# Kernel optimization log

Hardware: AMD Instinct MI355X
Metric: run time of the kernel (lower is better)

The kernel has to match this reference:

```python
import jax, jax.numpy as jnp
import numpy as np

WS = 3          # window_size == patch size (asserted in the torch forward)
R = WS // 2
V = WS ** 3     # 27 voxels per patch == window length
D_MODEL = 256
HEADS = 8
LAYERS = 3

_IDX = np.arange(WS)[:, None] + np.arange(WS)[None, :]  # [WS, WS] sliding-window indices into padded grid


def _layer_norm(x, g, b, eps=1e-5):
    mu = jnp.mean(x, axis=-1, keepdims=True)
    var = jnp.var(x, axis=-1, keepdims=True)
    return (x - mu) * jax.lax.rsqrt(var + eps) * g + b


def _gather_windows(x):
    # x: [B, WS, WS, WS, C] -> zero-padded 3x3x3 neighborhoods, [B*V, V, C]
    xp = jnp.pad(x, ((0, 0), (R, R), (R, R), (R, R), (0, 0)))
    nb = xp[:, _IDX][:, :, :, _IDX][:, :, :, :, :, _IDX]
    # axes: [B, d_ctr, d_win, h_ctr, h_win, w_ctr, w_win, C]
    nb = nb.transpose(0, 1, 3, 5, 2, 4, 6, 7)
    return nb.reshape(x.shape[0] * V, V, x.shape[-1])


def _window_mask(known_mask):
    # boundary (padding) positions -> False; interior -> known_mask value
    mp = jnp.pad(known_mask, ((0, 0), (R, R), (R, R), (R, R)))
    m = mp[:, _IDX][:, :, :, _IDX][:, :, :, :, :, _IDX]
    m = m.transpose(0, 1, 3, 5, 2, 4, 6)
    return m.reshape(known_mask.shape[0] * V, V)


def _forward(neighbors_patch, known_mask, w_in, b_in, pos_embed,
             ln1_g, ln1_b, ln2_g, ln2_b,
             Wq, bq, Wk, bk, Wv, bv, Wo, bo,
             W1, b1, W2, b2, w_out, b_out):
    B = neighbors_patch.shape[0]
    d = w_in.shape[0]
    hd = d // HEADS
    scale = hd ** -0.5
    # Conv3d(1, d, kernel_size=1) == per-voxel affine scalar -> d channels; then +pos_embed
    x = neighbors_patch[:, 0, :, :, :, None] * w_in + b_in + pos_embed  # [B,WS,WS,WS,d]
    mask = _window_mask(known_mask)  # [B*V, V] (constant across layers)
    N = B * V
    t = x.reshape(N, d)
    for l in range(LAYERS):
        # NOTE: K/V come from RAW (un-normed) neighbor embeddings, Q from norm1(target) - as in the torch code
        nb = _gather_windows(t.reshape(B, WS, WS, WS, d))  # [N, V, d]
        tn = _layer_norm(t, ln1_g[l], ln1_b[l])
        q = (tn @ Wq[l] + bq[l]).reshape(N, HEADS, hd)
        k = (nb @ Wk[l] + bk[l]).reshape(N, V, HEADS, hd)
        v = (nb @ Wv[l] + bv[l]).reshape(N, V, HEADS, hd)
        s = jnp.einsum('nhd,nlhd->nhl', q, k) * scale
        s = jnp.where(mask[:, None, :], s, -1e30)
        # fully-masked rows: torch softmax gives NaN then zeroed; here uniform*mask -> 0, same result
        a = jax.nn.softmax(s, axis=-1) * mask[:, None, :]
        o = jnp.einsum('nhl,nlhd->nhd', a, v).reshape(N, d) @ Wo[l] + bo[l]
        t = t + o  # dropout is identity in eval
        tn2 = _layer_norm(t, ln2_g[l], ln2_b[l])
        h = jax.nn.gelu(tn2 @ W1[l] + b1[l], approximate=False)
        t = t + h @ W2[l] + b2[l]
    center = t.reshape(B, WS, WS, WS, d)[:, R, R, R, :]
    return (center @ w_out)[:, None] + b_out  # [B, 1]


def setup_inputs():
    key = jax.random.key(0)
    ks = jax.random.split(key, 24)
    B, d, L, ff = 256, D_MODEL, LAYERS, 4 * D_MODEL
    nrm = lambda k, shape, s=0.02: jax.random.normal(k, shape, jnp.float32) * s
    return {
        'neighbors_patch': (jax.random.uniform(ks[0], (B, 1, WS, WS, WS)) < 0.5).astype(jnp.float32),
        'known_mask': jax.random.randint(ks[1], (B, WS, WS, WS), 0, 2).astype(bool),
        'w_in': nrm(ks[2], (d,), 0.5), 'b_in': nrm(ks[3], (d,)),
        'pos_embed': nrm(ks[4], (WS, WS, WS, d)),
        'ln1_g': jnp.ones((L, d)), 'ln1_b': jnp.zeros((L, d)),
        'ln2_g': jnp.ones((L, d)), 'ln2_b': jnp.zeros((L, d)),
        'Wq': nrm(ks[5], (L, d, d)), 'bq': nrm(ks[6], (L, d)),
        'Wk': nrm(ks[7], (L, d, d)), 'bk': nrm(ks[8], (L, d)),
        'Wv': nrm(ks[9], (L, d, d)), 'bv': nrm(ks[10], (L, d)),
        'Wo': nrm(ks[11], (L, d, d)), 'bo': nrm(ks[12], (L, d)),
        'W1': nrm(ks[13], (L, d, ff)), 'b1': nrm(ks[14], (L, ff)),
        'W2': nrm(ks[15], (L, ff, d)), 'b2': nrm(ks[16], (L, d)),
        'w_out': nrm(ks[17], (d,)), 'b_out': nrm(ks[18], (1,)),
    }


def reference(neighbors_patch, known_mask, w_in, b_in, pos_embed, ln1_g, ln1_b, ln2_g, ln2_b, Wq, bq, Wk, bk, Wv, bv, Wo, bo, W1, b1, W2, b2, w_out, b_out):
    return _forward(neighbors_patch, known_mask, w_in, b_in, pos_embed, ln1_g, ln1_b, ln2_g, ln2_b, Wq, bq, Wk, bk, Wv, bv, Wo, bo, W1, b1, W2, b2, w_out, b_out)
```

## Files before the change

### kernel.cpp

```cpp
#include <hip/hip_runtime.h>
#include <hip/hip_bf16.h>


#define NTOK 6912
#define DM   256
#define FF   1024

typedef __hip_bfloat16 bf16;
typedef __bf16 bf16x8 __attribute__((ext_vector_type(8)));
typedef float  f32x4  __attribute__((ext_vector_type(4)));

__device__ __forceinline__ void gload_lds16(const void* g, void* l) {
    __builtin_amdgcn_global_load_lds(
        (const __attribute__((address_space(1))) void*)g,
        (__attribute__((address_space(3))) void*)l, 16, 0, 0);
}

__device__ __forceinline__ unsigned short f2bf_bits(float x) {
    bf16 h = __float2bfloat16(x);
    union { bf16 h; unsigned short u; } c; c.h = h; return c.u;
}

__global__ __launch_bounds__(256) void embed_kernel(
    const float* __restrict__ npat, const float* __restrict__ w_in,
    const float* __restrict__ b_in, const float* __restrict__ pos,
    float* __restrict__ t, bf16* __restrict__ t_bf)
{
    int n = blockIdx.x;
    int c = threadIdx.x;
    int p = n % 27;
    float v = npat[n] * w_in[c] + b_in[c] + pos[p * DM + c];
    t[(size_t)n * DM + c] = v;
    t_bf[(size_t)n * DM + c] = __float2bfloat16(v);
}

__global__ void make_mask_kernel(const int* __restrict__ km,
                                 unsigned int* __restrict__ mask27)
{
    int n = blockIdx.x * blockDim.x + threadIdx.x;
    if (n >= NTOK) return;
    int b = n / 27, q = n % 27;
    int zq = q / 9, yq = (q / 3) % 3, xq = q % 3;
    unsigned int mb = 0u;
    for (int m = 0; m < 27; ++m) {
        int zm = m / 9, ym = (m / 3) % 3, xm = m % 3;
        if (abs(zm - zq) <= 1 && abs(ym - yq) <= 1 && abs(xm - xq) <= 1 &&
            km[b * 27 + m] != 0)
            mb |= (1u << m);
    }
    mask27[n] = mb;
}

__global__ __launch_bounds__(256) void convert_weights(
    const float* __restrict__ Wq, const float* __restrict__ Wk,
    const float* __restrict__ Wv, const float* __restrict__ Wo,
    const float* __restrict__ W1, const float* __restrict__ W2,
    bf16* __restrict__ Wt)
{
    __shared__ float tile[32][33];
    int id = blockIdx.z;
    int l = id / 6, wsel = id % 6;
    const float* src; bf16* dst; int K, N;
    if (wsel < 4) {
        const float* tbl[4] = {Wq, Wk, Wv, Wo};
        src = tbl[wsel] + (size_t)l * 65536; K = 256; N = 256;
        dst = Wt + (size_t)l * 786432 + wsel * 65536;
    } else if (wsel == 4) {
        src = W1 + (size_t)l * 262144; K = 256; N = 1024;
        dst = Wt + (size_t)l * 786432 + 262144;
    } else {
        src = W2 + (size_t)l * 262144; K = 1024; N = 256;
        dst = Wt + (size_t)l * 786432 + 524288;
    }
    int n0 = blockIdx.x * 32, k0 = blockIdx.y * 32;
    if (n0 >= N || k0 >= K) return;
    int tx = threadIdx.x, ty = threadIdx.y;
#pragma unroll
    for (int i = 0; i < 4; ++i)
        tile[ty + i * 8][tx] = src[(size_t)(k0 + ty + i * 8) * N + n0 + tx];
    __syncthreads();
#pragma unroll
    for (int i = 0; i < 4; ++i)
        dst[(size_t)(n0 + ty + i * 8) * K + k0 + tx] =
            __float2bfloat16(tile[tx][ty + i * 8]);
}

__global__ __launch_bounds__(256) void layernorm_kernel(
    const float* __restrict__ X, const float* __restrict__ g,
    const float* __restrict__ bta, bf16* __restrict__ Y)
{
    int n = blockIdx.x;
    int c = threadIdx.x;
    float x = X[(size_t)n * DM + c];
    float s = x, s2 = x * x;
    for (int off = 32; off; off >>= 1) {
        s  += __shfl_xor(s, off);
        s2 += __shfl_xor(s2, off);
    }
    __shared__ float ps[4], ps2[4];
    int w = c >> 6;
    if ((c & 63) == 0) { ps[w] = s; ps2[w] = s2; }
    __syncthreads();
    s  = ps[0] + ps[1] + ps[2] + ps[3];
    s2 = ps2[0] + ps2[1] + ps2[2] + ps2[3];
    float mu  = s * (1.0f / DM);
    float var = s2 * (1.0f / DM) - mu * mu;
    float r = rsqrtf(var + 1e-5f);
    Y[(size_t)n * DM + c] = __float2bfloat16((x - mu) * r * g[c] + bta[c]);
}

__device__ __forceinline__ void gemm_body(
    const bf16* __restrict__ A, const bf16* __restrict__ Bt,
    const float* __restrict__ bias, const float* __restrict__ residual,
    float* __restrict__ Cf, bf16* __restrict__ Cb,
    int K, int Nc, int act, int mode, int row0, int col0,
    bf16* As, bf16* Bs)
{
    int tid = threadIdx.x;
    int wv = tid >> 6, ln = tid & 63;
    int wr = wv >> 1, wc = wv & 1;

    f32x4 acc[4][2];
#pragma unroll
    for (int m = 0; m < 4; ++m)
#pragma unroll
        for (int n = 0; n < 2; ++n) acc[m][n] = (f32x4){0.f, 0.f, 0.f, 0.f};

    int lrow = ln >> 3;
    int kof  = (ln & 7) * 8;

    for (int k0 = 0; k0 < K; k0 += 64) {
        __syncthreads();
#pragma unroll
        for (int i = 0; i < 4; ++i) {
            int slot = i * 4 + wv;
            gload_lds16(A + (size_t)(row0 + slot * 8 + lrow) * K + k0 + kof,
                        As + slot * 512);
        }
#pragma unroll
        for (int i = 0; i < 2; ++i) {
            int slot = i * 4 + wv;
            gload_lds16(Bt + (size_t)(col0 + slot * 8 + lrow) * K + k0 + kof,
                        Bs + slot * 512);
        }
        __syncthreads();
        int lr = ln & 15, kg = ln >> 4;
#pragma unroll
        for (int kk = 0; kk < 2; ++kk) {
            int koff = kk * 32 + kg * 8;
            bf16x8 a[4], b[2];
#pragma unroll
            for (int m = 0; m < 4; ++m)
                a[m] = *(const bf16x8*)&As[(wr * 64 + m * 16 + lr) * 64 + koff];
#pragma unroll
            for (int n = 0; n < 2; ++n)
                b[n] = *(const bf16x8*)&Bs[(wc * 32 + n * 16 + lr) * 64 + koff];
#pragma unroll
            for (int m = 0; m < 4; ++m)
#pragma unroll
                for (int n = 0; n < 2; ++n)
                    acc[m][n] = __builtin_amdgcn_mfma_f32_16x16x32_bf16(
                        a[m], b[n], acc[m][n], 0, 0, 0);
        }
    }

    int lr = ln & 15, rg = ln >> 4;
#pragma unroll
    for (int m = 0; m < 4; ++m) {
#pragma unroll
        for (int n = 0; n < 2; ++n) {
            int col = col0 + wc * 32 + n * 16 + lr;
            float bcol = bias[col];
#pragma unroll
            for (int r = 0; r < 4; ++r) {
                int row = row0 + wr * 64 + m * 16 + rg * 4 + r;
                float v = acc[m][n][r] + bcol;
                if (mode == 2) {
                    int bb = row / 27, tok = row - bb * 27;
                    Cb[((size_t)bb * DM + col) * 32 + tok] = __float2bfloat16(v);
                } else {
                    size_t idx = (size_t)row * Nc + col;
                    if (residual) v += residual[idx];
                    if (act) v = 0.5f * v * (1.0f + erff(v * 0.70710678118654752f));
                    if (Cf) Cf[idx] = v;
                    if (Cb) Cb[idx] = __float2bfloat16(v);
                }
            }
        }
    }
}

__global__ __launch_bounds__(256) void gemm_bf16(
    const bf16* __restrict__ A, const bf16* __restrict__ Bt,
    const float* __restrict__ bias, const float* __restrict__ residual,
    float* __restrict__ Cf, bf16* __restrict__ Cb,
    int K, int Nc, int act)
{
    __shared__ __align__(16) bf16 As[128 * 64];
    __shared__ __align__(16) bf16 Bs[64 * 64];
    gemm_body(A, Bt, bias, residual, Cf, Cb, K, Nc, act, 0,
              blockIdx.x * 128, blockIdx.y * 64, As, Bs);
}

__global__ __launch_bounds__(256) void qkv_gemm(
    const bf16* __restrict__ tn, const bf16* __restrict__ tb,
    const bf16* __restrict__ wq,
    const float* __restrict__ bq, const float* __restrict__ bk,
    const float* __restrict__ bv,
    bf16* __restrict__ Qb, bf16* __restrict__ Kb, bf16* __restrict__ Vt)
{
    __shared__ __align__(16) bf16 As[128 * 64];
    __shared__ __align__(16) bf16 Bs[64 * 64];
    int ysel = blockIdx.y >> 2, ycol = blockIdx.y & 3;
    const bf16* A = (ysel == 0) ? tn : tb;
    const bf16* W = wq + (size_t)ysel * 65536;
    const float* bias = (ysel == 0) ? bq : (ysel == 1) ? bk : bv;
    bf16* Out = (ysel == 0) ? Qb : (ysel == 1) ? Kb : Vt;
    int mode = (ysel == 2) ? 2 : 0;
    gemm_body(A, W, bias, nullptr, nullptr, Out, DM, DM, 0, mode,
              blockIdx.x * 128, ycol * 64, As, Bs);
}

__global__ __launch_bounds__(256) void attention_mfma(
    const bf16* __restrict__ Qb, const bf16* __restrict__ Kb,
    const bf16* __restrict__ Vt, const unsigned int* __restrict__ mask27,
    bf16* __restrict__ out)
{
    __shared__ __align__(16) bf16 P_lds[4][32 * 40];
    int b  = blockIdx.x;
    int wv = threadIdx.x >> 6;
    int head = blockIdx.y * 4 + wv;
    int ln = threadIdx.x & 63;
    int r = ln & 15, g = ln >> 4;

    const bf16* Kp = Kb + (size_t)b * 27 * DM + head * 32;
    const bf16* Qp = Qb + (size_t)b * 27 * DM + head * 32;

    bf16x8 aK[2], bQ[2];
    aK[0] = *(const bf16x8*)(Kp + (size_t)r * DM + g * 8);
    aK[1] = *(const bf16x8*)(Kp + (size_t)(16 + r) * DM + g * 8);
    bQ[0] = *(const bf16x8*)(Qp + (size_t)r * DM + g * 8);
    bQ[1] = *(const bf16x8*)(Qp + (size_t)(16 + r) * DM + g * 8);

    f32x4 acc[2][2];
#pragma unroll
    for (int at = 0; at < 2; ++at)
#pragma unroll
        for (int bt = 0; bt < 2; ++bt)
            acc[at][bt] = __builtin_amdgcn_mfma_f32_16x16x32_bf16(
                aK[at], bQ[bt], (f32x4){0.f, 0.f, 0.f, 0.f}, 0, 0, 0);

    unsigned int Mq[2];
    Mq[0] = mask27[b * 27 + r];
    Mq[1] = (16 + r < 27) ? mask27[b * 27 + 16 + r] : 0u;

#pragma unroll
    for (int bt = 0; bt < 2; ++bt) {
        float e[2][4];
        float mx = -1e30f;
#pragma unroll
        for (int at = 0; at < 2; ++at)
#pragma unroll
            for (int rg = 0; rg < 4; ++rg) {
                int m = at * 16 + g * 4 + rg;
                bool in = (Mq[bt] >> m) & 1;
                float sv = acc[at][bt][rg] * 0.17677669529663687f;
                e[at][rg] = in ? sv : -1e30f;
                mx = fmaxf(mx, e[at][rg]);
            }
        mx = fmaxf(mx, __shfl_xor(mx, 16));
        mx = fmaxf(mx, __shfl_xor(mx, 32));
        float sum = 0.f;
#pragma unroll
        for (int at = 0; at < 2; ++at)
#pragma unroll
            for (int rg = 0; rg < 4; ++rg) {
                int m = at * 16 + g * 4 + rg;
                bool in = (Mq[bt] >> m) & 1;
                float ev = in ? expf(e[at][rg] - mx) : 0.f;
                e[at][rg] = ev;
                sum += ev;
            }
        sum += __shfl_xor(sum, 16);
        sum += __shfl_xor(sum, 32);
        float inv = (sum > 0.f) ? 1.f / sum : 0.f;
#pragma unroll
        for (int at = 0; at < 2; ++at) {
            ushort4 u;
            u.x = f2bf_bits(e[at][0] * inv);
            u.y = f2bf_bits(e[at][1] * inv);
            u.z = f2bf_bits(e[at][2] * inv);
            u.w = f2bf_bits(e[at][3] * inv);
            *(ushort4*)&P_lds[wv][(bt * 16 + r) * 40 + at * 16 + g * 4] = u;
        }
    }

    bf16x8 pa[2], vb[2];
    pa[0] = *(const bf16x8*)&P_lds[wv][(size_t)r * 40 + g * 8];
    pa[1] = *(const bf16x8*)&P_lds[wv][(size_t)(16 + r) * 40 + g * 8];
    const bf16* Vp = Vt + ((size_t)b * DM + head * 32) * 32;
    vb[0] = *(const bf16x8*)(Vp + (size_t)r * 32 + g * 8);
    vb[1] = *(const bf16x8*)(Vp + (size_t)(16 + r) * 32 + g * 8);

    f32x4 o[2][2];
#pragma unroll
    for (int qt = 0; qt < 2; ++qt)
#pragma unroll
        for (int dt = 0; dt < 2; ++dt)
            o[qt][dt] = __builtin_amdgcn_mfma_f32_16x16x32_bf16(
                pa[qt], vb[dt], (f32x4){0.f, 0.f, 0.f, 0.f}, 0, 0, 0);

#pragma unroll
    for (int qt = 0; qt < 2; ++qt)
#pragma unroll
        for (int dt = 0; dt < 2; ++dt)
#pragma unroll
            for (int rg = 0; rg < 4; ++rg) {
                int q = qt * 16 + g * 4 + rg;
                if (q < 27)
                    out[(size_t)(b * 27 + q) * DM + head * 32 + dt * 16 + r] =
                        __float2bfloat16(o[qt][dt][rg]);
            }
}

__global__ __launch_bounds__(256) void out_proj_kernel(
    const float* __restrict__ t, const float* __restrict__ w_out,
    const float* __restrict__ b_out, float* __restrict__ out)
{
    int bb = blockIdx.x;
    int c = threadIdx.x;
    float v = t[(size_t)(bb * 27 + 13) * DM + c] * w_out[c];
    for (int off = 32; off; off >>= 1) v += __shfl_xor(v, off);
    __shared__ float ps[4];
    if ((c & 63) == 0) ps[c >> 6] = v;
    __syncthreads();
    if (c == 0) out[bb] = ps[0] + ps[1] + ps[2] + ps[3] + b_out[0];
}

extern "C" void kernel_launch(void* const* d_in, const int* in_sizes, int n_in,
                              void* d_out, int out_size, void* d_ws, size_t ws_size,
                              hipStream_t stream)
{
    const float* npat  = (const float*)d_in[0];
    const int*   kmask = (const int*)  d_in[1];
    const float* w_in  = (const float*)d_in[2];
    const float* b_in  = (const float*)d_in[3];
    const float* pos   = (const float*)d_in[4];
    const float* ln1_g = (const float*)d_in[5];
    const float* ln1_b = (const float*)d_in[6];
    const float* ln2_g = (const float*)d_in[7];
    const float* ln2_b = (const float*)d_in[8];
    const float* Wq    = (const float*)d_in[9];
    const float* bq    = (const float*)d_in[10];
    const float* Wk    = (const float*)d_in[11];
    const float* bk    = (const float*)d_in[12];
    const float* Wv    = (const float*)d_in[13];
    const float* bv    = (const float*)d_in[14];
    const float* Wo    = (const float*)d_in[15];
    const float* bo    = (const float*)d_in[16];
    const float* W1    = (const float*)d_in[17];
    const float* b1    = (const float*)d_in[18];
    const float* W2    = (const float*)d_in[19];
    const float* b2    = (const float*)d_in[20];
    const float* w_out = (const float*)d_in[21];
    const float* b_out = (const float*)d_in[22];
    float* out = (float*)d_out;

    char* ws = (char*)d_ws;
    size_t f32mat = (size_t)NTOK * DM * 4;
    size_t bfmat  = (size_t)NTOK * DM * 2;
    float* t = (float*)(ws);
    char* p = ws + f32mat;
    bf16* t_bf   = (bf16*)(p);               p += bfmat;
    bf16* tn_bf  = (bf16*)(p);               p += bfmat;
    bf16* attn_bf= (bf16*)(p);               p += bfmat;
    bf16* Qb     = (bf16*)(p);               p += bfmat;
    bf16* Kb     = (bf16*)(p);               p += bfmat;
    bf16* Vt     = (bf16*)(p);               p += (size_t)256 * DM * 32 * 2;
    bf16* H_bf   = (bf16*)(p);               p += (size_t)NTOK * FF * 2;
    bf16* Wt     = (bf16*)(p);               p += (size_t)3 * 786432 * 2;
    unsigned int* mask27 = (unsigned int*)(p);

    convert_weights<<<dim3(32, 32, 18), dim3(32, 8), 0, stream>>>(
        Wq, Wk, Wv, Wo, W1, W2, Wt);
    embed_kernel<<<NTOK, 256, 0, stream>>>(npat, w_in, b_in, pos, t, t_bf);
    make_mask_kernel<<<(NTOK + 255) / 256, 256, 0, stream>>>(kmask, mask27);

    dim3 gDD(NTOK / 128, DM / 64);
    dim3 gQKV(NTOK / 128, 12);
    dim3 gFF(NTOK / 128, FF / 64);

    for (int l = 0; l < 3; ++l) {
        const bf16* wqt = Wt + (size_t)l * 786432;
        const bf16* wot = wqt + 3 * 65536;
        const bf16* w1t = wot + 65536;
        const bf16* w2t = w1t + 262144;

        layernorm_kernel<<<NTOK, 256, 0, stream>>>(t, ln1_g + l * DM, ln1_b + l * DM, tn_bf);
        qkv_gemm<<<gQKV, 256, 0, stream>>>(tn_bf, t_bf, wqt,
                                           bq + l * DM, bk + l * DM, bv + l * DM,
                                           Qb, Kb, Vt);
        attention_mfma<<<dim3(256, 2), 256, 0, stream>>>(Qb, Kb, Vt, mask27, attn_bf);
        gemm_bf16<<<gDD, 256, 0, stream>>>(attn_bf, wot, bo + l * DM, t, t, t_bf, DM, DM, 0);
        layernorm_kernel<<<NTOK, 256, 0, stream>>>(t, ln2_g + l * DM, ln2_b + l * DM, tn_bf);
        gemm_bf16<<<gFF, 256, 0, stream>>>(tn_bf, w1t, b1 + l * FF, nullptr, nullptr, H_bf, DM, FF, 1);
        gemm_bf16<<<gDD, 256, 0, stream>>>(H_bf, w2t, b2 + l * DM, t, t, t_bf, FF, DM, 0);
    }

    out_proj_kernel<<<256, 256, 0, stream>>>(t, w_out, b_out, out);
}
```

Baseline: 391.4 us.

## Fuse whole three-layer patch transformer into one persistent per-patch kernel

```diff
diff --git a/kernel.cpp b/kernel.cpp
--- a/kernel.cpp
+++ b/kernel.cpp
@@ -10,45 +10,16 @@
 typedef __bf16 bf16x8 __attribute__((ext_vector_type(8)));
 typedef float  f32x4  __attribute__((ext_vector_type(4)));
 
-__device__ __forceinline__ void gload_lds16(const void* g, void* l) {
-    __builtin_amdgcn_global_load_lds(
-        (const __attribute__((address_space(1))) void*)g,
-        (__attribute__((address_space(3))) void*)l, 16, 0, 0);
-}
-
 __device__ __forceinline__ unsigned short f2bf_bits(float x) {
     bf16 h = __float2bfloat16(x);
-    union { bf16 h; unsigned short u; } c; c.h = h; return c.u;
-}
-
-__global__ __launch_bounds__(256) void embed_kernel(
-    const float* __restrict__ npat, const float* __restrict__ w_in,
-    const float* __restrict__ b_in, const float* __restrict__ pos,
-    float* __restrict__ t, bf16* __restrict__ t_bf)
-{
-    int n = blockIdx.x;
-    int c = threadIdx.x;
-    int p = n % 27;
-    float v = npat[n] * w_in[c] + b_in[c] + pos[p * DM + c];
-    t[(size_t)n * DM + c] = v;
-    t_bf[(size_t)n * DM + c] = __float2bfloat16(v);
-}
-
-__global__ void make_mask_kernel(const int* __restrict__ km,
-                                 unsigned int* __restrict__ mask27)
-{
-    int n = blockIdx.x * blockDim.x + threadIdx.x;
-    if (n >= NTOK) return;
-    int b = n / 27, q = n % 27;
-    int zq = q / 9, yq = (q / 3) % 3, xq = q % 3;
-    unsigned int mb = 0u;
-    for (int m = 0; m < 27; ++m) {
-        int zm = m / 9, ym = (m / 3) % 3, xm = m % 3;
-        if (abs(zm - zq) <= 1 && abs(ym - yq) <= 1 && abs(xm - xq) <= 1 &&
-            km[b * 27 + m] != 0)
-            mb |= (1u << m);
-    }
-    mask27[n] = mb;
+    union { bf16 h; unsigned short u; } u2; u2.h = h; return u2.u;
+}
+
+__device__ __forceinline__ bf16x8 ldsA(const char* buf, int row, int kbyte, int rowB) {
+    return *(const bf16x8*)(buf + row * rowB + (kbyte ^ ((row & 7) << 4)));
+}
+__device__ __forceinline__ void ldsW(char* buf, int row, int col, int rowB, float v) {
+    *(unsigned short*)(buf + row * rowB + ((col * 2) ^ ((row & 7) << 4))) = f2bf_bits(v);
 }
 
 __global__ __launch_bounds__(256) void convert_weights(
@@ -85,256 +56,352 @@
             __float2bfloat16(tile[tx][ty + i * 8]);
 }
 
-__global__ __launch_bounds__(256) void layernorm_kernel(
-    const float* __restrict__ X, const float* __restrict__ g,
-    const float* __restrict__ bta, bf16* __restrict__ Y)
+template<int K, int ROWB>
+__device__ __forceinline__ void gemm32(const char* A, const bf16* __restrict__ Bt,
+                                       int wva, int c, int g, f32x4 acc[2][2])
 {
-    int n = blockIdx.x;
-    int c = threadIdx.x;
-    float x = X[(size_t)n * DM + c];
-    float s = x, s2 = x * x;
-    for (int off = 32; off; off >>= 1) {
-        s  += __shfl_xor(s, off);
-        s2 += __shfl_xor(s2, off);
-    }
-    __shared__ float ps[4], ps2[4];
-    int w = c >> 6;
-    if ((c & 63) == 0) { ps[w] = s; ps2[w] = s2; }
+#pragma unroll
+    for (int m = 0; m < 2; ++m)
+#pragma unroll
+        for (int n = 0; n < 2; ++n) acc[m][n] = (f32x4){0.f, 0.f, 0.f, 0.f};
+#pragma unroll
+    for (int ks = 0; ks < K / 32; ++ks) {
+        bf16x8 a0 = ldsA(A, c,      ks * 64 + g * 16, ROWB);
+        bf16x8 a1 = ldsA(A, 16 + c, ks * 64 + g * 16, ROWB);
+        const bf16* bp = Bt + (size_t)(wva * 32 + c) * K + ks * 32 + g * 8;
+        bf16x8 b0 = *(const bf16x8*)bp;
+        bf16x8 b1 = *(const bf16x8*)(bp + (size_t)16 * K);
+        acc[0][0] = __builtin_amdgcn_mfma_f32_16x16x32_bf16(a0, b0, acc[0][0], 0, 0, 0);
+        acc[0][1] = __builtin_amdgcn_mfma_f32_16x16x32_bf16(a0, b1, acc[0][1], 0, 0, 0);
+        acc[1][0] = __builtin_amdgcn_mfma_f32_16x16x32_bf16(a1, b0, acc[1][0], 0, 0, 0);
+        acc[1][1] = __builtin_amdgcn_mfma_f32_16x16x32_bf16(a1, b1, acc[1][1], 0, 0, 0);
+    }
+}
+
+__device__ __forceinline__ void ln_stats(const float tr[2][2][4], int wva, int c, int g,
+                                         float* red, float* red2,
+                                         float mu[2][4], float rr[2][4])
+{
+#pragma unroll
+    for (int m = 0; m < 2; ++m)
+#pragma unroll
+    for (int j = 0; j < 4; ++j) {
+        float s = tr[m][0][j] + tr[m][1][j];
+        float q = tr[m][0][j] * tr[m][0][j] + tr[m][1][j] * tr[m][1][j];
+#pragma unroll
+        for (int off = 1; off < 16; off <<= 1) {
+            s += __shfl_xor(s, off); q += __shfl_xor(q, off);
+        }
+        if (c == 0) { int row = m * 16 + g * 4 + j; red[row * 12 + wva] = s; red2[row * 12 + wva] = q; }
+    }
     __syncthreads();
-    s  = ps[0] + ps[1] + ps[2] + ps[3];
-    s2 = ps2[0] + ps2[1] + ps2[2] + ps2[3];
-    float mu  = s * (1.0f / DM);
-    float var = s2 * (1.0f / DM) - mu * mu;
-    float r = rsqrtf(var + 1e-5f);
-    Y[(size_t)n * DM + c] = __float2bfloat16((x - mu) * r * g[c] + bta[c]);
-}
-
-__device__ __forceinline__ void gemm_body(
-    const bf16* __restrict__ A, const bf16* __restrict__ Bt,
-    const float* __restrict__ bias, const float* __restrict__ residual,
-    float* __restrict__ Cf, bf16* __restrict__ Cb,
-    int K, int Nc, int act, int mode, int row0, int col0,
-    bf16* As, bf16* Bs)
+#pragma unroll
+    for (int m = 0; m < 2; ++m)
+#pragma unroll
+    for (int j = 0; j < 4; ++j) {
+        int row = m * 16 + g * 4 + j;
+        float S = 0.f, Q = 0.f;
+#pragma unroll
+        for (int w = 0; w < 8; ++w) { S += red[row * 12 + w]; Q += red2[row * 12 + w]; }
+        float m_ = S * (1.0f / DM);
+        float v_ = Q * (1.0f / DM) - m_ * m_;
+        mu[m][j] = m_; rr[m][j] = rsqrtf(v_ + 1e-5f);
+    }
+}
+
+__global__ __launch_bounds__(512, 2) void patch_net(
+    const float* __restrict__ npat, const int* __restrict__ km,
+    const float* __restrict__ w_in, const float* __restrict__ b_in,
+    const float* __restrict__ pos,
+    const float* __restrict__ ln1g, const float* __restrict__ ln1b,
+    const float* __restrict__ ln2g, const float* __restrict__ ln2b,
+    const float* __restrict__ bq, const float* __restrict__ bk,
+    const float* __restrict__ bv, const float* __restrict__ bo,
+    const float* __restrict__ b1, const float* __restrict__ b2,
+    const float* __restrict__ w_out, const float* __restrict__ b_out,
+    const bf16* __restrict__ Wt, float* __restrict__ out)
 {
+    __shared__ __align__(16) char L[110592];
+    char* Tbf = L;
+    char* Qb  = L + 16384;
+    char* Kb  = L + 32768;
+    char* Vt  = L + 49152;
+    char* Hb  = L;
+    char* TnA = L + 69632;
+    char* Pb  = L + 86016;
+    float* red  = (float*)(L + 106496);
+    float* red2 = (float*)(L + 108032);
+    unsigned* kbits_p = (unsigned*)(L + 109568);
+
+    int p = blockIdx.x;
     int tid = threadIdx.x;
-    int wv = tid >> 6, ln = tid & 63;
-    int wr = wv >> 1, wc = wv & 1;
-
-    f32x4 acc[4][2];
-#pragma unroll
-    for (int m = 0; m < 4; ++m)
-#pragma unroll
-        for (int n = 0; n < 2; ++n) acc[m][n] = (f32x4){0.f, 0.f, 0.f, 0.f};
-
-    int lrow = ln >> 3;
-    int kof  = (ln & 7) * 8;
-
-    for (int k0 = 0; k0 < K; k0 += 64) {
-        __syncthreads();
-#pragma unroll
-        for (int i = 0; i < 4; ++i) {
-            int slot = i * 4 + wv;
-            gload_lds16(A + (size_t)(row0 + slot * 8 + lrow) * K + k0 + kof,
-                        As + slot * 512);
-        }
-#pragma unroll
-        for (int i = 0; i < 2; ++i) {
-            int slot = i * 4 + wv;
-            gload_lds16(Bt + (size_t)(col0 + slot * 8 + lrow) * K + k0 + kof,
-                        Bs + slot * 512);
-        }
-        __syncthreads();
-        int lr = ln & 15, kg = ln >> 4;
-#pragma unroll
-        for (int kk = 0; kk < 2; ++kk) {
-            int koff = kk * 32 + kg * 8;
-            bf16x8 a[4], b[2];
-#pragma unroll
-            for (int m = 0; m < 4; ++m)
-                a[m] = *(const bf16x8*)&As[(wr * 64 + m * 16 + lr) * 64 + koff];
-#pragma unroll
-            for (int n = 0; n < 2; ++n)
-                b[n] = *(const bf16x8*)&Bs[(wc * 32 + n * 16 + lr) * 64 + koff];
-#pragma unroll
-            for (int m = 0; m < 4; ++m)
-#pragma unroll
-                for (int n = 0; n < 2; ++n)
-                    acc[m][n] = __builtin_amdgcn_mfma_f32_16x16x32_bf16(
-                        a[m], b[n], acc[m][n], 0, 0, 0);
-        }
-    }
-
-    int lr = ln & 15, rg = ln >> 4;
-#pragma unroll
-    for (int m = 0; m < 4; ++m) {
-#pragma unroll
-        for (int n = 0; n < 2; ++n) {
-            int col = col0 + wc * 32 + n * 16 + lr;
-            float bcol = bias[col];
-#pragma unroll
-            for (int r = 0; r < 4; ++r) {
-                int row = row0 + wr * 64 + m * 16 + rg * 4 + r;
-                float v = acc[m][n][r] + bcol;
-                if (mode == 2) {
-                    int bb = row / 27, tok = row - bb * 27;
-                    Cb[((size_t)bb * DM + col) * 32 + tok] = __float2bfloat16(v);
-                } else {
-                    size_t idx = (size_t)row * Nc + col;
-                    if (residual) v += residual[idx];
-                    if (act) v = 0.5f * v * (1.0f + erff(v * 0.70710678118654752f));
-                    if (Cf) Cf[idx] = v;
-                    if (Cb) Cb[idx] = __float2bfloat16(v);
+    int wva = tid >> 6, ln = tid & 63;
+    int c = ln & 15, g = ln >> 4;
+
+    unsigned win0 = 0, win1 = 0;
+    {
+        int zq0 = c / 9, yq0 = (c / 3) % 3, xq0 = c % 3;
+        int q1 = 16 + c, zq1 = q1 / 9, yq1 = (q1 / 3) % 3, xq1 = q1 % 3;
+        for (int m = 0; m < 27; ++m) {
+            int zm = m / 9, ym = (m / 3) % 3, xm = m % 3;
+            if (abs(zm - zq0) <= 1 && abs(ym - yq0) <= 1 && abs(xm - xq0) <= 1) win0 |= 1u << m;
+            if (q1 < 27 && abs(zm - zq1) <= 1 && abs(ym - yq1) <= 1 && abs(xm - xq1) <= 1) win1 |= 1u << m;
+        }
+    }
+    if (tid < 64) {
+        bool bit = (tid < 27) && (km[p * 27 + tid] != 0);
+        unsigned long long bm = __ballot(bit);
+        if (tid == 0) *kbits_p = (unsigned)(bm & 0x7FFFFFFull);
+    }
+
+    float tr[2][2][4];
+#pragma unroll
+    for (int m = 0; m < 2; ++m)
+#pragma unroll
+    for (int j = 0; j < 4; ++j) {
+        int row = m * 16 + g * 4 + j;
+        float nv = (row < 27) ? npat[p * 27 + row] : 0.f;
+#pragma unroll
+        for (int n = 0; n < 2; ++n) {
+            int col = wva * 32 + n * 16 + c;
+            float v = 0.f;
+            if (row < 27) v = nv * w_in[col] + b_in[col] + pos[row * DM + col];
+            tr[m][n][j] = v;
+            ldsW(Tbf, row, col, 512, v);
+        }
+    }
+
+    f32x4 acc[2][2];
+    float mu[2][4], rr[2][4];
+
+    for (int l = 0; l < 3; ++l) {
+        const bf16* wq  = Wt + (size_t)l * 786432;
+        const bf16* wk  = wq + 65536;
+        const bf16* wv2 = wk + 65536;
+        const bf16* wo  = wv2 + 65536;
+        const bf16* w1  = wo + 65536;
+        const bf16* w2  = w1 + 262144;
+
+        ln_stats(tr, wva, c, g, red, red2, mu, rr);
+#pragma unroll
+        for (int m = 0; m < 2; ++m)
+#pragma unroll
+        for (int j = 0; j < 4; ++j) {
+            int row = m * 16 + g * 4 + j;
+#pragma unroll
+            for (int n = 0; n < 2; ++n) {
+                int col = wva * 32 + n * 16 + c;
+                float v = (tr[m][n][j] - mu[m][j]) * rr[m][j] * ln1g[l * DM + col] + ln1b[l * DM + col];
+                ldsW(TnA, row, col, 512, v);
+            }
+        }
+        __syncthreads();
+
+        gemm32<256, 512>(TnA, wq, wva, c, g, acc);
+#pragma unroll
+        for (int m = 0; m < 2; ++m)
+#pragma unroll
+        for (int n = 0; n < 2; ++n) {
+            int col = wva * 32 + n * 16 + c; float bb = bq[l * DM + col];
+#pragma unroll
+            for (int j = 0; j < 4; ++j) ldsW(Qb, m * 16 + g * 4 + j, col, 512, acc[m][n][j] + bb);
+        }
+        gemm32<256, 512>(Tbf, wk, wva, c, g, acc);
+#pragma unroll
+        for (int m = 0; m < 2; ++m)
+#pragma unroll
+        for (int n = 0; n < 2; ++n) {
+            int col = wva * 32 + n * 16 + c; float bb = bk[l * DM + col];
+#pragma unroll
+            for (int j = 0; j < 4; ++j) ldsW(Kb, m * 16 + g * 4 + j, col, 512, acc[m][n][j] + bb);
+        }
+        gemm32<256, 512>(Tbf, wv2, wva, c, g, acc);
+#pragma unroll
+        for (int m = 0; m < 2; ++m)
+#pragma unroll
+        for (int n = 0; n < 2; ++n) {
+            int col = wva * 32 + n * 16 + c; float bb = bv[l * DM + col];
+#pragma unroll
+            for (int j = 0; j < 4; ++j)
+                *(unsigned short*)(Vt + col * 80 + (m * 16 + g * 4 + j) * 2) =
+                    f2bf_bits(acc[m][n][j] + bb);
+        }
+        __syncthreads();
+
+        {
+            int h = wva;
+            bf16x8 aK[2], bQ[2];
+#pragma unroll
+            for (int m = 0; m < 2; ++m) aK[m] = ldsA(Kb, m * 16 + c, h * 64 + g * 16, 512);
+#pragma unroll
+            for (int q = 0; q < 2; ++q) bQ[q] = ldsA(Qb, q * 16 + c, h * 64 + g * 16, 512);
+            f32x4 sA[2][2];
+#pragma unroll
+            for (int at = 0; at < 2; ++at)
+#pragma unroll
+            for (int bt = 0; bt < 2; ++bt)
+                sA[at][bt] = __builtin_amdgcn_mfma_f32_16x16x32_bf16(
+                    aK[at], bQ[bt], (f32x4){0.f, 0.f, 0.f, 0.f}, 0, 0, 0);
+
+            unsigned kb = *kbits_p;
+            unsigned Mq[2] = { kb & win0, kb & win1 };
+            char* Pw = Pb + wva * 2560;
+#pragma unroll
+            for (int bt = 0; bt < 2; ++bt) {
+                float e[2][4];
+                float mx = -1e30f;
+#pragma unroll
+                for (int at = 0; at < 2; ++at)
+#pragma unroll
+                for (int rg = 0; rg < 4; ++rg) {
+                    int m = at * 16 + g * 4 + rg;
+                    bool in = (Mq[bt] >> m) & 1;
+                    float sv = sA[at][bt][rg] * 0.17677669529663687f;
+                    e[at][rg] = in ? sv : -1e30f;
+                    mx = fmaxf(mx, e[at][rg]);
+                }
+                mx = fmaxf(mx, __shfl_xor(mx, 16));
+                mx = fmaxf(mx, __shfl_xor(mx, 32));
+                float sum = 0.f;
+#pragma unroll
+                for (int at = 0; at < 2; ++at)
+#pragma unroll
+                for (int rg = 0; rg < 4; ++rg) {
+                    int m = at * 16 + g * 4 + rg;
+                    bool in = (Mq[bt] >> m) & 1;
+                    float ev = in ? expf(e[at][rg] - mx) : 0.f;
+                    e[at][rg] = ev; sum += ev;
+                }
+                sum += __shfl_xor(sum, 16);
+                sum += __shfl_xor(sum, 32);
+                float inv = (sum > 0.f) ? 1.f / sum : 0.f;
+#pragma unroll
+                for (int at = 0; at < 2; ++at) {
+                    ushort4 u;
+                    u.x = f2bf_bits(e[at][0] * inv); u.y = f2bf_bits(e[at][1] * inv);
+                    u.z = f2bf_bits(e[at][2] * inv); u.w = f2bf_bits(e[at][3] * inv);
+                    *(ushort4*)(Pw + (bt * 16 + c) * 80 + (at * 16 + g * 4) * 2) = u;
                 }
             }
-        }
-    }
-}
-
-__global__ __launch_bounds__(256) void gemm_bf16(
-    const bf16* __restrict__ A, const bf16* __restrict__ Bt,
-    const float* __restrict__ bias, const float* __restrict__ residual,
-    float* __restrict__ Cf, bf16* __restrict__ Cb,
-    int K, int Nc, int act)
-{
-    __shared__ __align__(16) bf16 As[128 * 64];
-    __shared__ __align__(16) bf16 Bs[64 * 64];
-    gemm_body(A, Bt, bias, residual, Cf, Cb, K, Nc, act, 0,
-              blockIdx.x * 128, blockIdx.y * 64, As, Bs);
-}
-
-__global__ __launch_bounds__(256) void qkv_gemm(
-    const bf16* __restrict__ tn, const bf16* __restrict__ tb,
-    const bf16* __restrict__ wq,
-    const float* __restrict__ bq, const float* __restrict__ bk,
-    const float* __restrict__ bv,
-    bf16* __restrict__ Qb, bf16* __restrict__ Kb, bf16* __restrict__ Vt)
-{
-    __shared__ __align__(16) bf16 As[128 * 64];
-    __shared__ __align__(16) bf16 Bs[64 * 64];
-    int ysel = blockIdx.y >> 2, ycol = blockIdx.y & 3;
-    const bf16* A = (ysel == 0) ? tn : tb;
-    const bf16* W = wq + (size_t)ysel * 65536;
-    const float* bias = (ysel == 0) ? bq : (ysel == 1) ? bk : bv;
-    bf16* Out = (ysel == 0) ? Qb : (ysel == 1) ? Kb : Vt;
-    int mode = (ysel == 2) ? 2 : 0;
-    gemm_body(A, W, bias, nullptr, nullptr, Out, DM, DM, 0, mode,
-              blockIdx.x * 128, ycol * 64, As, Bs);
-}
-
-__global__ __launch_bounds__(256) void attention_mfma(
-    const bf16* __restrict__ Qb, const bf16* __restrict__ Kb,
-    const bf16* __restrict__ Vt, const unsigned int* __restrict__ mask27,
-    bf16* __restrict__ out)
-{
-    __shared__ __align__(16) bf16 P_lds[4][32 * 40];
-    int b  = blockIdx.x;
-    int wv = threadIdx.x >> 6;
-    int head = blockIdx.y * 4 + wv;
-    int ln = threadIdx.x & 63;
-    int r = ln & 15, g = ln >> 4;
-
-    const bf16* Kp = Kb + (size_t)b * 27 * DM + head * 32;
-    const bf16* Qp = Qb + (size_t)b * 27 * DM + head * 32;
-
-    bf16x8 aK[2], bQ[2];
-    aK[0] = *(const bf16x8*)(Kp + (size_t)r * DM + g * 8);
-    aK[1] = *(const bf16x8*)(Kp + (size_t)(16 + r) * DM + g * 8);
-    bQ[0] = *(const bf16x8*)(Qp + (size_t)r * DM + g * 8);
-    bQ[1] = *(const bf16x8*)(Qp + (size_t)(16 + r) * DM + g * 8);
-
-    f32x4 acc[2][2];
-#pragma unroll
-    for (int at = 0; at < 2; ++at)
-#pragma unroll
-        for (int bt = 0; bt < 2; ++bt)
-            acc[at][bt] = __builtin_amdgcn_mfma_f32_16x16x32_bf16(
-                aK[at], bQ[bt], (f32x4){0.f, 0.f, 0.f, 0.f}, 0, 0, 0);
-
-    unsigned int Mq[2];
-    Mq[0] = mask27[b * 27 + r];
-    Mq[1] = (16 + r < 27) ? mask27[b * 27 + 16 + r] : 0u;
-
-#pragma unroll
-    for (int bt = 0; bt < 2; ++bt) {
-        float e[2][4];
-        float mx = -1e30f;
-#pragma unroll
-        for (int at = 0; at < 2; ++at)
-#pragma unroll
-            for (int rg = 0; rg < 4; ++rg) {
-                int m = at * 16 + g * 4 + rg;
-                bool in = (Mq[bt] >> m) & 1;
-                float sv = acc[at][bt][rg] * 0.17677669529663687f;
-                e[at][rg] = in ? sv : -1e30f;
-                mx = fmaxf(mx, e[at][rg]);
+            bf16x8 pa[2], vb[2];
+#pragma unroll
+            for (int qt = 0; qt < 2; ++qt) pa[qt] = *(const bf16x8*)(Pw + (qt * 16 + c) * 80 + g * 16);
+#pragma unroll
+            for (int dt = 0; dt < 2; ++dt)
+                vb[dt] = *(const bf16x8*)(Vt + (h * 32 + dt * 16 + c) * 80 + g * 16);
+            f32x4 o[2][2];
+#pragma unroll
+            for (int qt = 0; qt < 2; ++qt)
+#pragma unroll
+            for (int dt = 0; dt < 2; ++dt)
+                o[qt][dt] = __builtin_amdgcn_mfma_f32_16x16x32_bf16(
+                    pa[qt], vb[dt], (f32x4){0.f, 0.f, 0.f, 0.f}, 0, 0, 0);
+#pragma unroll
+            for (int qt = 0; qt < 2; ++qt)
+#pragma unroll
+            for (int dt = 0; dt < 2; ++dt)
+#pragma unroll
+            for (int rg = 0; rg < 4; ++rg)
+                ldsW(TnA, qt * 16 + g * 4 + rg, h * 32 + dt * 16 + c, 512, o[qt][dt][rg]);
+        }
+        __syncthreads();
+
+        gemm32<256, 512>(TnA, wo, wva, c, g, acc);
+#pragma unroll
+        for (int m = 0; m < 2; ++m)
+#pragma unroll
+        for (int n = 0; n < 2; ++n) {
+            int col = wva * 32 + n * 16 + c; float bb = bo[l * DM + col];
+#pragma unroll
+            for (int j = 0; j < 4; ++j) tr[m][n][j] += acc[m][n][j] + bb;
+        }
+
+        ln_stats(tr, wva, c, g, red, red2, mu, rr);
+#pragma unroll
+        for (int m = 0; m < 2; ++m)
+#pragma unroll
+        for (int j = 0; j < 4; ++j) {
+            int row = m * 16 + g * 4 + j;
+#pragma unroll
+            for (int n = 0; n < 2; ++n) {
+                int col = wva * 32 + n * 16 + c;
+                float v = (tr[m][n][j] - mu[m][j]) * rr[m][j] * ln2g[l * DM + col] + ln2b[l * DM + col];
+                ldsW(TnA, row, col, 512, v);
             }
-        mx = fmaxf(mx, __shfl_xor(mx, 16));
-        mx = fmaxf(mx, __shfl_xor(mx, 32));
-        float sum = 0.f;
-#pragma unroll
-        for (int at = 0; at < 2; ++at)
-#pragma unroll
-            for (int rg = 0; rg < 4; ++rg) {
-                int m = at * 16 + g * 4 + rg;
-                bool in = (Mq[bt] >> m) & 1;
-                float ev = in ? expf(e[at][rg] - mx) : 0.f;
-                e[at][rg] = ev;
-                sum += ev;
+        }
+        __syncthreads();
+
+        {
+            f32x4 a8[2][8];
+#pragma unroll
+            for (int m = 0; m < 2; ++m)
+#pragma unroll
+            for (int n = 0; n < 8; ++n) a8[m][n] = (f32x4){0.f, 0.f, 0.f, 0.f};
+#pragma unroll
+            for (int ks = 0; ks < 8; ++ks) {
+                bf16x8 a0 = ldsA(TnA, c,      ks * 64 + g * 16, 512);
+                bf16x8 a1 = ldsA(TnA, 16 + c, ks * 64 + g * 16, 512);
+#pragma unroll
+                for (int n = 0; n < 8; ++n) {
+                    const bf16* bp = w1 + (size_t)(wva * 128 + n * 16 + c) * 256 + ks * 32 + g * 8;
+                    bf16x8 b0 = *(const bf16x8*)bp;
+                    a8[0][n] = __builtin_amdgcn_mfma_f32_16x16x32_bf16(a0, b0, a8[0][n], 0, 0, 0);
+                    a8[1][n] = __builtin_amdgcn_mfma_f32_16x16x32_bf16(a1, b0, a8[1][n], 0, 0, 0);
+                }
             }
-        sum += __shfl_xor(sum, 16);
-        sum += __shfl_xor(sum, 32);
-        float inv = (sum > 0.f) ? 1.f / sum : 0.f;
-#pragma unroll
-        for (int at = 0; at < 2; ++at) {
-            ushort4 u;
-            u.x = f2bf_bits(e[at][0] * inv);
-            u.y = f2bf_bits(e[at][1] * inv);
-            u.z = f2bf_bits(e[at][2] * inv);
-            u.w = f2bf_bits(e[at][3] * inv);
-            *(ushort4*)&P_lds[wv][(bt * 16 + r) * 40 + at * 16 + g * 4] = u;
-        }
-    }
-
-    bf16x8 pa[2], vb[2];
-    pa[0] = *(const bf16x8*)&P_lds[wv][(size_t)r * 40 + g * 8];
-    pa[1] = *(const bf16x8*)&P_lds[wv][(size_t)(16 + r) * 40 + g * 8];
-    const bf16* Vp = Vt + ((size_t)b * DM + head * 32) * 32;
-    vb[0] = *(const bf16x8*)(Vp + (size_t)r * 32 + g * 8);
-    vb[1] = *(const bf16x8*)(Vp + (size_t)(16 + r) * 32 + g * 8);
-
-    f32x4 o[2][2];
-#pragma unroll
-    for (int qt = 0; qt < 2; ++qt)
-#pragma unroll
-        for (int dt = 0; dt < 2; ++dt)
-            o[qt][dt] = __builtin_amdgcn_mfma_f32_16x16x32_bf16(
-                pa[qt], vb[dt], (f32x4){0.f, 0.f, 0.f, 0.f}, 0, 0, 0);
-
-#pragma unroll
-    for (int qt = 0; qt < 2; ++qt)
-#pragma unroll
-        for (int dt = 0; dt < 2; ++dt)
-#pragma unroll
-            for (int rg = 0; rg < 4; ++rg) {
-                int q = qt * 16 + g * 4 + rg;
-                if (q < 27)
-                    out[(size_t)(b * 27 + q) * DM + head * 32 + dt * 16 + r] =
-                        __float2bfloat16(o[qt][dt][rg]);
+#pragma unroll
+            for (int m = 0; m < 2; ++m)
+#pragma unroll
+            for (int n = 0; n < 8; ++n) {
+                int col = wva * 128 + n * 16 + c;
+                float bb = b1[l * FF + col];
+#pragma unroll
+                for (int j = 0; j < 4; ++j) {
+                    float v = a8[m][n][j] + bb;
+                    v = 0.5f * v * (1.0f + erff(v * 0.70710678118654752f));
+                    ldsW(Hb, m * 16 + g * 4 + j, col, 2048, v);
+                }
             }
-}
-
-__global__ __launch_bounds__(256) void out_proj_kernel(
-    const float* __restrict__ t, const float* __restrict__ w_out,
-    const float* __restrict__ b_out, float* __restrict__ out)
-{
-    int bb = blockIdx.x;
-    int c = threadIdx.x;
-    float v = t[(size_t)(bb * 27 + 13) * DM + c] * w_out[c];
-    for (int off = 32; off; off >>= 1) v += __shfl_xor(v, off);
-    __shared__ float ps[4];
-    if ((c & 63) == 0) ps[c >> 6] = v;
+        }
+        __syncthreads();
+
+        gemm32<1024, 2048>(Hb, w2, wva, c, g, acc);
+#pragma unroll
+        for (int m = 0; m < 2; ++m)
+#pragma unroll
+        for (int n = 0; n < 2; ++n) {
+            int col = wva * 32 + n * 16 + c; float bb = b2[l * DM + col];
+#pragma unroll
+            for (int j = 0; j < 4; ++j) tr[m][n][j] += acc[m][n][j] + bb;
+        }
+        __syncthreads();
+
+#pragma unroll
+        for (int m = 0; m < 2; ++m)
+#pragma unroll
+        for (int j = 0; j < 4; ++j) {
+            int row = m * 16 + g * 4 + j;
+#pragma unroll
+            for (int n = 0; n < 2; ++n)
+                ldsW(Tbf, row, wva * 32 + n * 16 + c, 512, tr[m][n][j]);
+        }
+        __syncthreads();
+    }
+
+    float v = 0.f;
+    if (g == 3) {
+        v = tr[0][0][1] * w_out[wva * 32 + c] + tr[0][1][1] * w_out[wva * 32 + 16 + c];
+    }
+#pragma unroll
+    for (int off = 1; off < 16; off <<= 1) v += __shfl_xor(v, off);
+    if (ln == 48) red[wva] = v;
     __syncthreads();
-    if (c == 0) out[bb] = ps[0] + ps[1] + ps[2] + ps[3] + b_out[0];
+    if (tid == 0) {
+        float s = 0.f;
+#pragma unroll
+        for (int w = 0; w < 8; ++w) s += red[w];
+        out[p] = s + b_out[0];
+    }
 }
 
 extern "C" void kernel_launch(void* const* d_in, const int* in_sizes, int n_in,
@@ -366,46 +433,11 @@
     const float* b_out = (const float*)d_in[22];
     float* out = (float*)d_out;
 
-    char* ws = (char*)d_ws;
-    size_t f32mat = (size_t)NTOK * DM * 4;
-    size_t bfmat  = (size_t)NTOK * DM * 2;
-    float* t = (float*)(ws);
-    char* p = ws + f32mat;
-    bf16* t_bf   = (bf16*)(p);               p += bfmat;
-    bf16* tn_bf  = (bf16*)(p);               p += bfmat;
-    bf16* attn_bf= (bf16*)(p);               p += bfmat;
-    bf16* Qb     = (bf16*)(p);               p += bfmat;
-    bf16* Kb     = (bf16*)(p);               p += bfmat;
-    bf16* Vt     = (bf16*)(p);               p += (size_t)256 * DM * 32 * 2;
-    bf16* H_bf   = (bf16*)(p);               p += (size_t)NTOK * FF * 2;
-    bf16* Wt     = (bf16*)(p);               p += (size_t)3 * 786432 * 2;
-    unsigned int* mask27 = (unsigned int*)(p);
+    bf16* Wt = (bf16*)d_ws;
 
     convert_weights<<<dim3(32, 32, 18), dim3(32, 8), 0, stream>>>(
         Wq, Wk, Wv, Wo, W1, W2, Wt);
-    embed_kernel<<<NTOK, 256, 0, stream>>>(npat, w_in, b_in, pos, t, t_bf);
-    make_mask_kernel<<<(NTOK + 255) / 256, 256, 0, stream>>>(kmask, mask27);
-
-    dim3 gDD(NTOK / 128, DM / 64);
-    dim3 gQKV(NTOK / 128, 12);
-    dim3 gFF(NTOK / 128, FF / 64);
-
-    for (int l = 0; l < 3; ++l) {
-        const bf16* wqt = Wt + (size_t)l * 786432;
-        const bf16* wot = wqt + 3 * 65536;
-        const bf16* w1t = wot + 65536;
-        const bf16* w2t = w1t + 262144;
-
-        layernorm_kernel<<<NTOK, 256, 0, stream>>>(t, ln1_g + l * DM, ln1_b + l * DM, tn_bf);
-        qkv_gemm<<<gQKV, 256, 0, stream>>>(tn_bf, t_bf, wqt,
-                                           bq + l * DM, bk + l * DM, bv + l * DM,
-                                           Qb, Kb, Vt);
-        attention_mfma<<<dim3(256, 2), 256, 0, stream>>>(Qb, Kb, Vt, mask27, attn_bf);
-        gemm_bf16<<<gDD, 256, 0, stream>>>(attn_bf, wot, bo + l * DM, t, t, t_bf, DM, DM, 0);
-        layernorm_kernel<<<NTOK, 256, 0, stream>>>(t, ln2_g + l * DM, ln2_b + l * DM, tn_bf);
-        gemm_bf16<<<gFF, 256, 0, stream>>>(tn_bf, w1t, b1 + l * FF, nullptr, nullptr, H_bf, DM, FF, 1);
-        gemm_bf16<<<gDD, 256, 0, stream>>>(H_bf, w2t, b2 + l * DM, t, t, t_bf, FF, DM, 0);
-    }
-
-    out_proj_kernel<<<256, 256, 0, stream>>>(t, w_out, b_out, out);
-}
+    patch_net<<<256, 512, 0, stream>>>(
+        npat, kmask, w_in, b_in, pos, ln1_g, ln1_b, ln2_g, ln2_b,
+        bq, bk, bv, bo, b1, b2, w_out, b_out, Wt, out);
+}
```

New measurement: 403.4 us. 1.03x slower.
